# Optimization experiments

Measured on AMD Instinct MI355X. Metric: run time of the kernel, lower is better.

## Reference

```python
import jax, jax.numpy as jnp
import numpy as np

N = 32       # number of variables (per-var LSTMs)
L = 128      # window length
D = 128      # hidden dim
HEADS = 8
TAU_MAX = 5
ALPHA = 0.7  # attn_decay_alpha
B = 128      # number of time-ordered windows


def setup_inputs() -> dict:
    key = jax.random.key(0)
    ks = jax.random.split(key, 20)
    s = 0.1
    f = lambda k, shape: (jax.random.normal(k, shape, jnp.float32) * s)
    return {
        "X": jax.random.normal(ks[0], (B, L, N), jnp.float32),
        # per-variable encoder LSTM (input size 1): W_ih (N,4D), W_hh (N,4D,D), combined-style biases kept separate
        "enc_Wih": f(ks[1], (N, 4 * D)),
        "enc_Whh": f(ks[2], (N, 4 * D, D)),
        "enc_b": f(ks[3], (N, 4 * D)),            # b_ih + b_hh merged (mathematically identical)
        "pool_w": f(ks[4], (N, D)),
        "pool_b": f(ks[5], (N,)),
        # shared MultiheadAttention params (torch layout: in_proj (3D,D))
        "in_proj_w": f(ks[6], (3 * D, D)),
        "in_proj_b": f(ks[7], (3 * D,)),
        "out_proj_w": f(ks[8], (D, D)),
        "out_proj_b": f(ks[9], (D,)),
        # per-variable decoder: init_h/init_c Linear(d,d), LSTM(1,d) (input is all-zeros so W_ih drops out), out Linear(d,1)
        "dec_initH_w": f(ks[10], (N, D, D)),
        "dec_initH_b": f(ks[11], (N, D)),
        "dec_initC_w": f(ks[12], (N, D, D)),
        "dec_initC_b": f(ks[13], (N, D)),
        "dec_Whh": f(ks[14], (N, 4 * D, D)),
        "dec_bih": f(ks[15], (N, 4 * D)),
        "dec_bhh": f(ks[16], (N, 4 * D)),
        "dec_out_w": f(ks[17], (N, D)),
        "dec_out_b": f(ks[18], (N,)),
    }


def _lstm_cell(gates, c):
    # torch gate order: i, f, g, o
    i, fg, g, o = jnp.split(gates, 4, axis=-1)
    i = jax.nn.sigmoid(i); fg = jax.nn.sigmoid(fg)
    g = jnp.tanh(g); o = jax.nn.sigmoid(o)
    c = fg * c + i * g
    h = o * jnp.tanh(c)
    return h, c


def _encode(X, Wih, Whh, b, pool_w, pool_b):
    # X: (B,L,N); encoder consumes first L-1 steps of each variable, batched over all N vars
    x = jnp.transpose(X[:, :-1, :], (1, 2, 0))  # (T, N, B)
    Bn = X.shape[0]
    h0 = jnp.zeros((N, Bn, D), X.dtype)

    def step(carry, x_t):  # x_t: (N,B)
        h, c = carry
        gates = (x_t[..., None] * Wih[:, None, :]
                 + jnp.einsum('nbd,ngd->nbg', h, Whh)
                 + b[:, None, :])
        h, c = _lstm_cell(gates, c)
        return (h, c), h

    _, H = jax.lax.scan(step, (h0, h0), x)  # H: (T,N,B,D)
    # TemporalAttnPool: softmax over time of a linear score, weighted sum
    scores = jnp.einsum('tnbd,nd->tnb', H, pool_w) + pool_b[None, :, None]
    a = jax.nn.softmax(scores, axis=0)
    C = jnp.einsum('tnb,tnbd->bnd', a, H)  # (B,N,D)
    return C


def _mha(Q, KV, in_w, in_b, out_w, out_b):
    dh = D // HEADS
    q = Q @ in_w[:D].T + in_b[:D]
    k = KV @ in_w[D:2 * D].T + in_b[D:2 * D]
    v = KV @ in_w[2 * D:].T + in_b[2 * D:]
    sp = lambda x: x.reshape(x.shape[0], x.shape[1], HEADS, dh)
    q, k, v = sp(q), sp(k), sp(v)
    scores = jnp.einsum('bqhd,bkhd->bhqk', q, k) / float(np.sqrt(dh))
    attn = jax.nn.softmax(scores, axis=-1)
    o = jnp.einsum('bhqk,bkhd->bqhd', attn, v).reshape(Q.shape)
    return o @ out_w.T + out_b


def _cross_attend(C, in_w, in_b, out_w, out_b):
    Bn = C.shape[0]
    tmax = min(TAU_MAX, Bn - 1)
    if tmax <= 0:
        return C
    out_sum = jnp.zeros_like(C)
    w_sum = jnp.zeros((Bn, 1, 1), C.dtype)
    for tau in range(1, tmax + 1):  # small fixed loop over lags
        o = _mha(C[tau:], C[:-tau], in_w, in_b, out_w, out_b)
        w = float(np.exp(-ALPHA * (tau - 1)))  # attn_agg == 'decay'
        out_sum = out_sum.at[tau:].add(o * w)
        w_sum = w_sum.at[tau:].add(w)
    out = out_sum / jnp.clip(w_sum, 1e-8)
    return C + out  # residual=True


def _decode(C_star, iHw, iHb, iCw, iCb, Whh, bih, bhh, ow, ob):
    # h0/c0 from tanh(Linear(c_star)); LSTM input is all-zeros so input term reduces to b_ih
    h0 = jnp.tanh(jnp.einsum('bnd,ned->nbe', C_star, iHw) + iHb[:, None, :])
    c0 = jnp.tanh(jnp.einsum('bnd,ned->nbe', C_star, iCw) + iCb[:, None, :])
    b = (bih + bhh)[:, None, :]  # (N,1,4D)

    def step(carry, _):
        h, c = carry
        gates = jnp.einsum('nbd,ngd->nbg', h, Whh) + b
        h, c = _lstm_cell(gates, c)
        o = jnp.einsum('nbd,nd->nb', h, ow) + ob[:, None]
        return (h, c), o

    _, O = jax.lax.scan(step, (h0, c0), None, length=L)  # (L,N,B)
    recon = jnp.transpose(O[:L - 1], (2, 0, 1))  # (B,L-1,N)
    pred = O[L - 1].T                            # (B,N)
    return recon, pred


def reference(X, enc_Wih, enc_Whh, enc_b, pool_w, pool_b,
              in_proj_w, in_proj_b, out_proj_w, out_proj_b,
              dec_initH_w, dec_initH_b, dec_initC_w, dec_initC_b,
              dec_Whh, dec_bih, dec_bhh, dec_out_w, dec_out_b):
    C = _encode(X, enc_Wih, enc_Whh, enc_b, pool_w, pool_b)
    C_star = _cross_attend(C, in_proj_w, in_proj_b, out_proj_w, out_proj_b)
    recon, pred = _decode(C_star, dec_initH_w, dec_initH_b, dec_initC_w, dec_initC_b,
                          dec_Whh, dec_bih, dec_bhh, dec_out_w, dec_out_b)
    return recon, pred, C_star
```

## Files before the change

kernel.cpp:

```cpp
#include <hip/hip_runtime.h>
#include <hip/hip_bf16.h>

typedef unsigned short ushort_t;
typedef unsigned int uint_t;

#define DD   128
#define G4   512
#define BT   16
#define NB   128
#define NV   32

#define OFF_WIH   0
#define OFF_EB    16384
#define OFF_PW    32768
#define OFF_PB    36864
#define OFF_INW   37120
#define OFF_INB   86272
#define OFF_OUTW  86784
#define OFF_OUTB  103168
#define OFF_IHB   103424
#define OFF_ICB   107520
#define OFF_DBIH  111616
#define OFF_DBHH  128000
#define OFF_DOW   144384
#define OFF_DOB   148480
#define P_TOTAL   148736

typedef __attribute__((ext_vector_type(8))) short bf16x8;
typedef __attribute__((ext_vector_type(4))) float f32x4;

__device__ __forceinline__ float bf2f(ushort_t u) {
    union { uint_t i; float f; } x; x.i = ((uint_t)u) << 16; return x.f;
}
__device__ __forceinline__ ushort_t f2bf(float f) {
    __hip_bfloat16 h = __float2bfloat16(f);
    return *(ushort_t*)&h;
}
__device__ __forceinline__ uint_t f2u(float f) {
    union { float f; uint_t i; } x; x.f = f; return x.i;
}
__device__ __forceinline__ float u2f(uint_t u) {
    union { uint_t i; float f; } x; x.i = u; return x.f;
}
__device__ __forceinline__ float sigmoid_f(float x) {
    return __builtin_amdgcn_rcpf(1.f + __expf(-x));
}
__device__ __forceinline__ float tanh_f(float x) {
    float e = __expf(2.f * x);
    return 1.f - 2.f * __builtin_amdgcn_rcpf(e + 1.f);
}
__device__ __forceinline__ float swz_bcast_l15(float v) {
    return u2f((uint_t)__builtin_amdgcn_ds_swizzle((int)f2u(v), 0x000F));
}
__device__ __forceinline__ void store_out(void* out, long idx, float v, int bf) {
    if (bf) ((ushort_t*)out)[idx] = f2bf(v);
    else    ((float*)out)[idx]    = v;
}
__device__ __forceinline__ int wave_probe(const void* p, int elems) {
    int cap = elems < 2048 ? elems : 2048;
    int lane = threadIdx.x & 63;
    const ushort_t* u = (const ushort_t*)p;
    int cnt = 0, tot = 0;
    for (int j = lane; j < cap; j += 64) {
        ushort_t x = u[j];
        float af = fabsf(bf2f(x));
        tot++;
        if (x == 0 || (af > 1e-7f && af < 100.f)) cnt++;
    }
    #pragma unroll
    for (int off = 32; off >= 1; off >>= 1) {
        cnt += __shfl_xor(cnt, off);
        tot += __shfl_xor(tot, off);
    }
    return (cnt * 10 >= tot * 9) ? 1 : 0;
}

struct Ptr19 { const void* p[19]; };

__global__ __launch_bounds__(256) void prep_kernel(Ptr19 a, float* __restrict__ P,
                                                   float* __restrict__ Xc) {
    __shared__ float tile[32][65];
    if (blockIdx.x < 581) {
        int base = blockIdx.x * 256;
        int src, o0, size;
        if      (base < OFF_EB)   { src = 1;  o0 = base - OFF_WIH;  size = 16384; }
        else if (base < OFF_PW)   { src = 3;  o0 = base - OFF_EB;   size = 16384; }
        else if (base < OFF_PB)   { src = 4;  o0 = base - OFF_PW;   size = 4096;  }
        else if (base < OFF_INW)  { src = 5;  o0 = base - OFF_PB;   size = 32;    }
        else if (base < OFF_INB)  { src = 6;  o0 = base - OFF_INW;  size = 49152; }
        else if (base < OFF_OUTW) { src = 7;  o0 = base - OFF_INB;  size = 384;   }
        else if (base < OFF_OUTB) { src = 8;  o0 = base - OFF_OUTW; size = 16384; }
        else if (base < OFF_IHB)  { src = 9;  o0 = base - OFF_OUTB; size = 128;   }
        else if (base < OFF_ICB)  { src = 11; o0 = base - OFF_IHB;  size = 4096;  }
        else if (base < OFF_DBIH) { src = 13; o0 = base - OFF_ICB;  size = 4096;  }
        else if (base < OFF_DBHH) { src = 15; o0 = base - OFF_DBIH; size = 16384; }
        else if (base < OFF_DOW)  { src = 16; o0 = base - OFF_DBHH; size = 16384; }
        else if (base < OFF_DOB)  { src = 17; o0 = base - OFF_DOW;  size = 4096;  }
        else                      { src = 18; o0 = base - OFF_DOB;  size = 32;    }
        int bf = wave_probe(a.p[src], size);
        int off = o0 + (int)threadIdx.x;
        if (off < size)
            P[base + threadIdx.x] = bf ? bf2f(((const ushort_t*)a.p[src])[off])
                                       : ((const float*)a.p[src])[off];
    } else {
        int bf = wave_probe(a.p[0], 2048);
        int idx2 = blockIdx.x - 581;
        int bt = (idx2 & 3) * 32, tn0 = (idx2 >> 2) * 64;
        const void* src = a.p[0];
        int tx = threadIdx.x & 63, ty = threadIdx.x >> 6;
        #pragma unroll
        for (int k = 0; k < 8; k++) {
            int row = ty * 8 + k;
            int idx = (bt + row) * 4096 + tn0 + tx;
            tile[row][tx] = bf ? bf2f(((const ushort_t*)src)[idx]) : ((const float*)src)[idx];
        }
        __syncthreads();
        int bx = threadIdx.x & 31, tyy = threadIdx.x >> 5;
        #pragma unroll
        for (int k = 0; k < 8; k++) {
            int tn = tn0 + tyy * 8 + k;
            int t = tn >> 5, nn = tn & 31;
            Xc[t * 4096 + nn * 128 + bt + bx] = tile[bx][tyy * 8 + k];
        }
    }
}

__global__ __launch_bounds__(512, 2) void enc_kernel(
    const float* __restrict__ Xc, const void* __restrict__ Wraw,
    const float* __restrict__ P, float* __restrict__ Cout)
{
    const int n = blockIdx.y, b0 = blockIdx.x * BT;
    const int tid = threadIdx.x;
    const int w = tid >> 6, lane = tid & 63;
    const int l15 = lane & 15, quad = lane >> 4;
    const int wbf = wave_probe(Wraw, 2048);
    const int bown = b0 + l15;

    __shared__ alignas(16) ushort_t hS[2][16 * 136];
    for (int i = tid; i < 16 * 136; i += 512) hS[0][i] = 0;

    bf16x8 afrag[4][4];
    #pragma unroll
    for (int typ = 0; typ < 4; typ++) {
        const int g = typ * 128 + 16 * w + l15;
        #pragma unroll
        for (int kc = 0; kc < 4; kc++) {
            const int base = (n * G4 + g) * DD + 32 * kc + 8 * quad;
            if (wbf) {
                afrag[typ][kc] = *(const bf16x8*)((const ushort_t*)Wraw + base);
            } else {
                const float* fp = (const float*)Wraw + base;
                bf16x8 tmp;
                #pragma unroll
                for (int j = 0; j < 8; j++) tmp[j] = (short)f2bf(fp[j]);
                afrag[typ][kc] = tmp;
            }
        }
    }

    bf16x8 pfrag[4];
    #pragma unroll
    for (int kc = 0; kc < 4; kc++) {
        bf16x8 tmp;
        #pragma unroll
        for (int j = 0; j < 8; j++)
            tmp[j] = (l15 == 0 || l15 == 8)
                   ? (short)f2bf(P[OFF_PW + n * DD + 32 * kc + 8 * quad + j]) : (short)0;
        pfrag[kc] = tmp;
    }

    f32x4 bias4[4], wih4[4];
    #pragma unroll
    for (int typ = 0; typ < 4; typ++) {
        int base = n * G4 + typ * 128 + 16 * w + 4 * quad;
        bias4[typ] = *(const f32x4*)&P[OFF_EB + base];
        wih4[typ]  = *(const f32x4*)&P[OFF_WIH + base];
    }
    const float pb_r = P[OFF_PB + n];

    float cst[4], hprev[4], Cacc[4], lR = 0.f;
    #pragma unroll
    for (int r = 0; r < 4; r++) { cst[r] = 0.f; hprev[r] = 0.f; Cacc[r] = 0.f; }

    float xq = Xc[n * 128 + bown];

#define ENC_STEP(T, RB)                                                              \
    do {                                                                             \
        __syncthreads();                                                             \
        bf16x8 bh[4];                                                                \
        _Pragma("unroll")                                                            \
        for (int kc = 0; kc < 4; kc++)                                               \
            bh[kc] = *(const bf16x8*)&hS[RB][l15 * 136 + 32 * kc + 8 * quad];        \
        f32x4 acc[4], accP;                                                          \
        _Pragma("unroll")                                                            \
        for (int typ = 0; typ < 4; typ++) {                                          \
            f32x4 a;                                                                 \
            a.x = bias4[typ].x + xq * wih4[typ].x;                                   \
            a.y = bias4[typ].y + xq * wih4[typ].y;                                   \
            a.z = bias4[typ].z + xq * wih4[typ].z;                                   \
            a.w = bias4[typ].w + xq * wih4[typ].w;                                   \
            acc[typ] = a;                                                            \
        }                                                                            \
        accP.x = pb_r; accP.y = pb_r; accP.z = pb_r; accP.w = pb_r;                  \
        if ((T) < 126) xq = Xc[((T) + 1) * 4096 + n * 128 + bown];                   \
        _Pragma("unroll")                                                            \
        for (int kc = 0; kc < 4; kc++) {                                             \
            accP = __builtin_amdgcn_mfma_f32_16x16x32_bf16(pfrag[kc], bh[kc], accP, 0, 0, 0); \
            _Pragma("unroll")                                                        \
            for (int typ = 0; typ < 4; typ++)                                        \
                acc[typ] = __builtin_amdgcn_mfma_f32_16x16x32_bf16(afrag[typ][kc], bh[kc], acc[typ], 0, 0, 0); \
        }                                                                            \
        if ((T) > 0) {                                                               \
            float e = __expf(swz_bcast_l15(accP[0]));                                \
            lR += e;                                                                 \
            _Pragma("unroll")                                                        \
            for (int r = 0; r < 4; r++) Cacc[r] = fmaf(e, hprev[r], Cacc[r]);        \
        }                                                                            \
        ushort4 hw;                                                                  \
        _Pragma("unroll")                                                            \
        for (int r = 0; r < 4; r++) {                                                \
            float ii = sigmoid_f(acc[0][r]);                                         \
            float ff = sigmoid_f(acc[1][r]);                                         \
            float g2 = tanh_f(acc[2][r]);                                            \
            float oo = sigmoid_f(acc[3][r]);                                         \
            float cc = ff * cst[r] + ii * g2;                                        \
            cst[r] = cc;                                                             \
            float hh = oo * tanh_f(cc);                                              \
            hprev[r] = hh;                                                           \
            ((ushort_t*)&hw)[r] = f2bf(hh);                                          \
        }                                                                            \
        *(ushort4*)&hS[(RB) ^ 1][l15 * 136 + 16 * w + 4 * quad] = hw;                \
    } while (0)

    for (int tp = 0; tp < 63; tp++) {
        ENC_STEP(2 * tp, 0);
        ENC_STEP(2 * tp + 1, 1);
    }
    ENC_STEP(126, 0);
#undef ENC_STEP

    __syncthreads();
    {
        f32x4 accP;
        accP.x = pb_r; accP.y = pb_r; accP.z = pb_r; accP.w = pb_r;
        #pragma unroll
        for (int kc = 0; kc < 4; kc++) {
            bf16x8 bh = *(const bf16x8*)&hS[1][l15 * 136 + 32 * kc + 8 * quad];
            accP = __builtin_amdgcn_mfma_f32_16x16x32_bf16(pfrag[kc], bh, accP, 0, 0, 0);
        }
        float e = __expf(swz_bcast_l15(accP[0]));
        lR += e;
        #pragma unroll
        for (int r = 0; r < 4; r++) Cacc[r] = fmaf(e, hprev[r], Cacc[r]);
    }
    float inv = 1.f / lR;
    f32x4 cv;
    cv.x = Cacc[0] * inv; cv.y = Cacc[1] * inv; cv.z = Cacc[2] * inv; cv.w = Cacc[3] * inv;
    *(f32x4*)&Cout[bown * (NV * DD) + n * DD + 16 * w + 4 * quad] = cv;
}

__global__ __launch_bounds__(256) void qkv_kernel(
    const float* __restrict__ C, const float* __restrict__ P,
    float* __restrict__ q, float* __restrict__ k, float* __restrict__ v)
{
    int b = blockIdx.x, p = blockIdx.y, tid = threadIdx.x;
    int j = tid & 127, half = tid >> 7;
    __shared__ float Cb[NV * DD];
    for (int i = tid; i < NV * DD; i += 256) Cb[i] = C[b * (NV * DD) + i];
    __syncthreads();

    const float* wrow = P + OFF_INW + (p * DD + j) * DD;
    float bias = P[OFF_INB + p * DD + j];
    float acc[16];
    #pragma unroll
    for (int nn = 0; nn < 16; nn++) acc[nn] = bias;

    for (int dc = 0; dc < DD; dc += 8) {
        float4 w0 = *(const float4*)&wrow[dc];
        float4 w1 = *(const float4*)&wrow[dc + 4];
        #pragma unroll
        for (int nn = 0; nn < 16; nn++) {
            const float* cb = &Cb[(half * 16 + nn) * DD + dc];
            float4 c0 = *(float4*)&cb[0];
            float4 c1 = *(float4*)&cb[4];
            acc[nn] += c0.x * w0.x + c0.y * w0.y + c0.z * w0.z + c0.w * w0.w
                     + c1.x * w1.x + c1.y * w1.y + c1.z * w1.z + c1.w * w1.w;
        }
    }
    float* dst = (p == 0) ? q : (p == 1) ? k : v;
    for (int nn = 0; nn < 16; nn++)
        dst[b * (NV * DD) + (half * 16 + nn) * DD + j] = acc[nn];
}

__global__ __launch_bounds__(256) void attn_kernel(
    const float* __restrict__ q, const float* __restrict__ k, const float* __restrict__ v,
    const float* __restrict__ C, const float* __restrict__ P,
    const void* __restrict__ Xraw, float* __restrict__ Cstar, void* __restrict__ dout)
{
    int b = blockIdx.x, tid = threadIdx.x;
    int obf = wave_probe(Xraw, 2048);
    __shared__ float Qs[NV * DD], Ks[NV * DD], Vs[NV * DD];
    float* Os = Ks;
    for (int i = tid; i < NV * DD; i += 256) Qs[i] = q[b * (NV * DD) + i];
    __syncthreads();

    int hh = tid >> 5, qi = tid & 31;
    float qreg[16];
    #pragma unroll
    for (int u = 0; u < 4; u++) {
        float4 t4 = *(float4*)&Qs[qi * DD + hh * 16 + 4 * u];
        qreg[4*u] = t4.x; qreg[4*u+1] = t4.y; qreg[4*u+2] = t4.z; qreg[4*u+3] = t4.w;
    }

    float Oacc[16];
    #pragma unroll
    for (int u = 0; u < 16; u++) Oacc[u] = 0.f;
    float wsum = 0.f;
    int tmax = (b < 5) ? b : 5;

    for (int tau = 1; tau <= tmax; tau++) {
        __syncthreads();
        for (int i = tid; i < NV * DD; i += 256) {
            Ks[i] = k[(b - tau) * (NV * DD) + i];
            Vs[i] = v[(b - tau) * (NV * DD) + i];
        }
        __syncthreads();

        float s[NV];
        #pragma unroll
        for (int kk = 0; kk < NV; kk++) {
            float a = 0.f;
            #pragma unroll
            for (int u = 0; u < 4; u++) {
                float4 kv = *(float4*)&Ks[kk * DD + hh * 16 + 4 * u];
                a += qreg[4*u] * kv.x + qreg[4*u+1] * kv.y
                   + qreg[4*u+2] * kv.z + qreg[4*u+3] * kv.w;
            }
            s[kk] = a * 0.25f;
        }
        float mm = s[0];
        #pragma unroll
        for (int kk = 1; kk < NV; kk++) mm = fmaxf(mm, s[kk]);
        float ssum = 0.f;
        #pragma unroll
        for (int kk = 0; kk < NV; kk++) { s[kk] = __expf(s[kk] - mm); ssum += s[kk]; }
        float wdk = __expf(-0.7f * (float)(tau - 1));
        wsum += wdk;
        float wr = wdk / ssum;
        #pragma unroll
        for (int u = 0; u < 4; u++) {
            float ax = 0.f, ay = 0.f, az = 0.f, aw = 0.f;
            #pragma unroll
            for (int kk = 0; kk < NV; kk++) {
                float4 vv = *(float4*)&Vs[kk * DD + hh * 16 + 4 * u];
                ax += s[kk] * vv.x; ay += s[kk] * vv.y;
                az += s[kk] * vv.z; aw += s[kk] * vv.w;
            }
            Oacc[4*u] += wr * ax; Oacc[4*u+1] += wr * ay;
            Oacc[4*u+2] += wr * az; Oacc[4*u+3] += wr * aw;
        }
    }

    __syncthreads();
    float winv = (b > 0) ? 1.f / wsum : 0.f;
    #pragma unroll
    for (int u = 0; u < 16; u++)
        Os[qi * DD + hh * 16 + u] = Oacc[u] * winv;
    __syncthreads();

    int j = tid & 127, ng = tid >> 7;
    const float* wrow = P + OFF_OUTW + j * DD;
    float obias = P[OFF_OUTB + j];
    for (int nn = ng * 16; nn < ng * 16 + 16; nn++) {
        float a = (b > 0) ? obias : 0.f;
        for (int dc = 0; dc < DD; dc += 8) {
            float4 w0 = *(const float4*)&wrow[dc];
            float4 w1 = *(const float4*)&wrow[dc + 4];
            float4 o0 = *(float4*)&Os[nn * DD + dc];
            float4 o1 = *(float4*)&Os[nn * DD + dc + 4];
            a += o0.x*w0.x + o0.y*w0.y + o0.z*w0.z + o0.w*w0.w
               + o1.x*w1.x + o1.y*w1.y + o1.z*w1.z + o1.w*w1.w;
        }
        float cs = C[b * (NV * DD) + nn * DD + j] + a;
        Cstar[b * (NV * DD) + nn * DD + j] = cs;
        store_out(dout, 524288 + b * (NV * DD) + nn * DD + j, cs, obf);
    }
}

__global__ __launch_bounds__(512, 2) void dec_kernel(
    const float* __restrict__ Cstar,
    const void* __restrict__ iHw, const void* __restrict__ iCw,
    const void* __restrict__ Wraw, const void* __restrict__ Xraw,
    const float* __restrict__ P, void* __restrict__ out)
{
    const int n = blockIdx.y, b0 = blockIdx.x * BT;
    const int tid = threadIdx.x;
    const int w = tid >> 6, lane = tid & 63;
    const int l15 = lane & 15, quad = lane >> 4;
    const int wbf = wave_probe(Wraw, 2048);
    const int obf = wave_probe(Xraw, 2048);
    const int hbf = wave_probe(iHw, 2048);
    const int cbf = wave_probe(iCw, 2048);
    const int bown = b0 + l15;

    __shared__ alignas(16) ushort_t hS[2][16 * 136];

    bf16x8 cstB[4];
    #pragma unroll
    for (int kc = 0; kc < 4; kc++) {
        const float* cp = &Cstar[bown * (NV * DD) + n * DD + 32 * kc + 8 * quad];
        f32x4 c0v = *(const f32x4*)&cp[0];
        f32x4 c1v = *(const f32x4*)&cp[4];
        bf16x8 tmp;
        tmp[0] = (short)f2bf(c0v.x); tmp[1] = (short)f2bf(c0v.y);
        tmp[2] = (short)f2bf(c0v.z); tmp[3] = (short)f2bf(c0v.w);
        tmp[4] = (short)f2bf(c1v.x); tmp[5] = (short)f2bf(c1v.y);
        tmp[6] = (short)f2bf(c1v.z); tmp[7] = (short)f2bf(c1v.w);
        cstB[kc] = tmp;
    }
    float cst[4];
    {
        f32x4 hAcc = *(const f32x4*)&P[OFF_IHB + n * DD + 16 * w + 4 * quad];
        f32x4 cAcc = *(const f32x4*)&P[OFF_ICB + n * DD + 16 * w + 4 * quad];
        #pragma unroll
        for (int kc = 0; kc < 4; kc++) {
            const int base = (n * DD + 16 * w + l15) * DD + 32 * kc + 8 * quad;
            bf16x8 wA;
            if (hbf) wA = *(const bf16x8*)((const ushort_t*)iHw + base);
            else {
                const float* fp = (const float*)iHw + base;
                #pragma unroll
                for (int j = 0; j < 8; j++) wA[j] = (short)f2bf(fp[j]);
            }
            hAcc = __builtin_amdgcn_mfma_f32_16x16x32_bf16(wA, cstB[kc], hAcc, 0, 0, 0);
            if (cbf) wA = *(const bf16x8*)((const ushort_t*)iCw + base);
            else {
                const float* fp = (const float*)iCw + base;
                #pragma unroll
                for (int j = 0; j < 8; j++) wA[j] = (short)f2bf(fp[j]);
            }
            cAcc = __builtin_amdgcn_mfma_f32_16x16x32_bf16(wA, cstB[kc], cAcc, 0, 0, 0);
        }
        ushort4 hw;
        #pragma unroll
        for (int r = 0; r < 4; r++) {
            ((ushort_t*)&hw)[r] = f2bf(tanh_f(hAcc[r]));
            cst[r] = tanh_f(cAcc[r]);
        }
        *(ushort4*)&hS[0][l15 * 136 + 16 * w + 4 * quad] = hw;
    }

    bf16x8 afrag[4][4];
    #pragma unroll
    for (int typ = 0; typ < 4; typ++) {
        const int g = typ * 128 + 16 * w + l15;
        #pragma unroll
        for (int kc = 0; kc < 4; kc++) {
            const int base = (n * G4 + g) * DD + 32 * kc + 8 * quad;
            if (wbf) {
                afrag[typ][kc] = *(const bf16x8*)((const ushort_t*)Wraw + base);
            } else {
                const float* fp = (const float*)Wraw + base;
                bf16x8 tmp;
                #pragma unroll
                for (int j = 0; j < 8; j++) tmp[j] = (short)f2bf(fp[j]);
                afrag[typ][kc] = tmp;
            }
        }
    }

    bf16x8 pfrag[4];
    #pragma unroll
    for (int kc = 0; kc < 4; kc++) {
        bf16x8 tmp;
        #pragma unroll
        for (int j = 0; j < 8; j++)
            tmp[j] = (l15 == 0) ? (short)f2bf(P[OFF_DOW + n * DD + 32 * kc + 8 * quad + j]) : (short)0;
        pfrag[kc] = tmp;
    }

    f32x4 bias4[4];
    #pragma unroll
    for (int typ = 0; typ < 4; typ++) {
        int base = n * G4 + typ * 128 + 16 * w + 4 * quad;
        f32x4 b1 = *(const f32x4*)&P[OFF_DBIH + base];
        f32x4 b2 = *(const f32x4*)&P[OFF_DBHH + base];
        bias4[typ].x = b1.x + b2.x; bias4[typ].y = b1.y + b2.y;
        bias4[typ].z = b1.z + b2.z; bias4[typ].w = b1.w + b2.w;
    }
    const float ob_r = P[OFF_DOB + n];

#define DEC_STEP(T, RB)                                                              \
    do {                                                                             \
        __syncthreads();                                                             \
        bf16x8 bh[4];                                                                \
        _Pragma("unroll")                                                            \
        for (int kc = 0; kc < 4; kc++)                                               \
            bh[kc] = *(const bf16x8*)&hS[RB][l15 * 136 + 32 * kc + 8 * quad];        \
        f32x4 acc[4];                                                                \
        _Pragma("unroll")                                                            \
        for (int typ = 0; typ < 4; typ++) acc[typ] = bias4[typ];                     \
        _Pragma("unroll")                                                            \
        for (int kc = 0; kc < 4; kc++)                                               \
            _Pragma("unroll")                                                        \
            for (int typ = 0; typ < 4; typ++)                                        \
                acc[typ] = __builtin_amdgcn_mfma_f32_16x16x32_bf16(afrag[typ][kc], bh[kc], acc[typ], 0, 0, 0); \
        if (w == 0) {                                                                \
            f32x4 accP;                                                              \
            accP.x = ob_r; accP.y = ob_r; accP.z = ob_r; accP.w = ob_r;              \
            _Pragma("unroll")                                                        \
            for (int kc = 0; kc < 4; kc++)                                           \
                accP = __builtin_amdgcn_mfma_f32_16x16x32_bf16(pfrag[kc], bh[kc], accP, 0, 0, 0); \
            if ((T) > 0 && quad == 0)                                                \
                store_out(out, (long)bown * 4064 + (long)((T) - 1) * NV + n, accP[0], obf); \
        }                                                                            \
        ushort4 hw;                                                                  \
        _Pragma("unroll")                                                            \
        for (int r = 0; r < 4; r++) {                                                \
            float ii = sigmoid_f(acc[0][r]);                                         \
            float ff = sigmoid_f(acc[1][r]);                                         \
            float g2 = tanh_f(acc[2][r]);                                            \
            float oo = sigmoid_f(acc[3][r]);                                         \
            float cc = ff * cst[r] + ii * g2;                                        \
            cst[r] = cc;                                                             \
            ((ushort_t*)&hw)[r] = f2bf(oo * tanh_f(cc));                             \
        }                                                                            \
        *(ushort4*)&hS[(RB) ^ 1][l15 * 136 + 16 * w + 4 * quad] = hw;                \
    } while (0)

    for (int tp = 0; tp < 64; tp++) {
        DEC_STEP(2 * tp, 0);
        DEC_STEP(2 * tp + 1, 1);
    }
#undef DEC_STEP

    __syncthreads();
    if (w == 0) {
        f32x4 accP;
        accP.x = ob_r; accP.y = ob_r; accP.z = ob_r; accP.w = ob_r;
        #pragma unroll
        for (int kc = 0; kc < 4; kc++) {
            bf16x8 bh = *(const bf16x8*)&hS[0][l15 * 136 + 32 * kc + 8 * quad];
            accP = __builtin_amdgcn_mfma_f32_16x16x32_bf16(pfrag[kc], bh, accP, 0, 0, 0);
        }
        if (quad == 0)
            store_out(out, 520192 + (long)bown * NV + n, accP[0], obf);
    }
}

extern "C" void kernel_launch(void* const* d_in, const int* in_sizes, int n_in,
                              void* d_out, int out_size, void* d_ws, size_t ws_size,
                              hipStream_t stream) {
    char* ws = (char*)d_ws;
    float*    P    = (float*)(ws + 0);
    float*    Xc   = (float*)(ws + (1u << 20));
    float*    C    = (float*)(ws + (3u << 20));
    float*    qb   = (float*)(ws + (5u << 20));
    float*    kb   = (float*)(ws + (7u << 20));
    float*    vb   = (float*)(ws + (9u << 20));
    float*    Cst  = (float*)(ws + (11u << 20));

    Ptr19 a;
    for (int i = 0; i < 19; i++) a.p[i] = d_in[i];

    prep_kernel<<<837, 256, 0, stream>>>(a, P, Xc);
    enc_kernel<<<dim3(8, 32), 512, 0, stream>>>(Xc, d_in[2], P, C);
    qkv_kernel<<<dim3(128, 3), 256, 0, stream>>>(C, P, qb, kb, vb);
    attn_kernel<<<128, 256, 0, stream>>>(qb, kb, vb, C, P, d_in[0], Cst, d_out);
    dec_kernel<<<dim3(8, 32), 512, 0, stream>>>(Cst, d_in[10], d_in[12], d_in[14], d_in[0], P, d_out);
}
```

Measured before the change: 436.1 us.

## Split MFMA accumulation chains and precompute dtype flags in prep kernel

The recurrent gate matmuls in the encoder and decoder now accumulate into two independent register chains (k-chunks 0-1 and 2-3) that are summed at the end. This shortens the dependent MFMA chain on the per-step critical path. The dtype probes that each block used to run on entry are computed once by five extra prep blocks and stored as flags in P. The pooling weight fragment is now replicated across all rows, so the swizzle broadcast of the attention logit can be dropped. The cost is extra accumulator registers and a few vector adds per step.

After: 448.4 us. 1.03x slower.

```diff
diff --git a/kernel.cpp b/kernel.cpp
--- a/kernel.cpp
+++ b/kernel.cpp
@@ -25,6 +25,7 @@
 #define OFF_DOW   144384
 #define OFF_DOB   148480
 #define P_TOTAL   148736
+#define OFF_FLAGS (OFF_PB + 32)
 
 typedef __attribute__((ext_vector_type(8))) short bf16x8;
 typedef __attribute__((ext_vector_type(4))) float f32x4;
@@ -36,21 +37,12 @@
     __hip_bfloat16 h = __float2bfloat16(f);
     return *(ushort_t*)&h;
 }
-__device__ __forceinline__ uint_t f2u(float f) {
-    union { float f; uint_t i; } x; x.f = f; return x.i;
-}
-__device__ __forceinline__ float u2f(uint_t u) {
-    union { uint_t i; float f; } x; x.i = u; return x.f;
-}
 __device__ __forceinline__ float sigmoid_f(float x) {
     return __builtin_amdgcn_rcpf(1.f + __expf(-x));
 }
 __device__ __forceinline__ float tanh_f(float x) {
     float e = __expf(2.f * x);
     return 1.f - 2.f * __builtin_amdgcn_rcpf(e + 1.f);
-}
-__device__ __forceinline__ float swz_bcast_l15(float v) {
-    return u2f((uint_t)__builtin_amdgcn_ds_swizzle((int)f2u(v), 0x000F));
 }
 __device__ __forceinline__ void store_out(void* out, long idx, float v, int bf) {
     if (bf) ((ushort_t*)out)[idx] = f2bf(v);
@@ -102,7 +94,7 @@
         if (off < size)
             P[base + threadIdx.x] = bf ? bf2f(((const ushort_t*)a.p[src])[off])
                                        : ((const float*)a.p[src])[off];
-    } else {
+    } else if (blockIdx.x < 837) {
         int bf = wave_probe(a.p[0], 2048);
         int idx2 = blockIdx.x - 581;
         int bt = (idx2 & 3) * 32, tn0 = (idx2 >> 2) * 64;
@@ -122,6 +114,12 @@
             int t = tn >> 5, nn = tn & 31;
             Xc[t * 4096 + nn * 128 + bt + bx] = tile[bx][tyy * 8 + k];
         }
+    } else {
+        int which = blockIdx.x - 837;
+        int src = (which == 0) ? 0 : (which == 1) ? 2 : (which == 2) ? 10
+                : (which == 3) ? 12 : 14;
+        int flag = wave_probe(a.p[src], 2048);
+        if (threadIdx.x == 0) P[OFF_FLAGS + which] = (float)flag;
     }
 }
 
@@ -133,7 +131,7 @@
     const int tid = threadIdx.x;
     const int w = tid >> 6, lane = tid & 63;
     const int l15 = lane & 15, quad = lane >> 4;
-    const int wbf = wave_probe(Wraw, 2048);
+    const int wbf = P[OFF_FLAGS + 1] > 0.5f;
     const int bown = b0 + l15;
 
     __shared__ alignas(16) ushort_t hS[2][16 * 136];
@@ -164,8 +162,7 @@
         bf16x8 tmp;
         #pragma unroll
         for (int j = 0; j < 8; j++)
-            tmp[j] = (l15 == 0 || l15 == 8)
-                   ? (short)f2bf(P[OFF_PW + n * DD + 32 * kc + 8 * quad + j]) : (short)0;
+            tmp[j] = (short)f2bf(P[OFF_PW + n * DD + 32 * kc + 8 * quad + j]);
         pfrag[kc] = tmp;
     }
 
@@ -191,7 +188,7 @@
         _Pragma("unroll")                                                            \
         for (int kc = 0; kc < 4; kc++)                                               \
             bh[kc] = *(const bf16x8*)&hS[RB][l15 * 136 + 32 * kc + 8 * quad];        \
-        f32x4 acc[4], accP;                                                          \
+        f32x4 acc[4], acc2[4], accP, accP2;                                          \
         _Pragma("unroll")                                                            \
         for (int typ = 0; typ < 4; typ++) {                                          \
             f32x4 a;                                                                 \
@@ -200,18 +197,29 @@
             a.z = bias4[typ].z + xq * wih4[typ].z;                                   \
             a.w = bias4[typ].w + xq * wih4[typ].w;                                   \
             acc[typ] = a;                                                            \
+            acc2[typ].x = 0.f; acc2[typ].y = 0.f; acc2[typ].z = 0.f; acc2[typ].w = 0.f; \
         }                                                                            \
         accP.x = pb_r; accP.y = pb_r; accP.z = pb_r; accP.w = pb_r;                  \
+        accP2.x = 0.f; accP2.y = 0.f; accP2.z = 0.f; accP2.w = 0.f;                  \
         if ((T) < 126) xq = Xc[((T) + 1) * 4096 + n * 128 + bown];                   \
         _Pragma("unroll")                                                            \
-        for (int kc = 0; kc < 4; kc++) {                                             \
+        for (int kc = 0; kc < 2; kc++) {                                             \
             accP = __builtin_amdgcn_mfma_f32_16x16x32_bf16(pfrag[kc], bh[kc], accP, 0, 0, 0); \
             _Pragma("unroll")                                                        \
             for (int typ = 0; typ < 4; typ++)                                        \
                 acc[typ] = __builtin_amdgcn_mfma_f32_16x16x32_bf16(afrag[typ][kc], bh[kc], acc[typ], 0, 0, 0); \
         }                                                                            \
+        _Pragma("unroll")                                                            \
+        for (int kc = 2; kc < 4; kc++) {                                             \
+            accP2 = __builtin_amdgcn_mfma_f32_16x16x32_bf16(pfrag[kc], bh[kc], accP2, 0, 0, 0); \
+            _Pragma("unroll")                                                        \
+            for (int typ = 0; typ < 4; typ++)                                        \
+                acc2[typ] = __builtin_amdgcn_mfma_f32_16x16x32_bf16(afrag[typ][kc], bh[kc], acc2[typ], 0, 0, 0); \
+        }                                                                            \
+        _Pragma("unroll")                                                            \
+        for (int typ = 0; typ < 4; typ++) acc[typ] = acc[typ] + acc2[typ];           \
         if ((T) > 0) {                                                               \
-            float e = __expf(swz_bcast_l15(accP[0]));                                \
+            float e = __expf(accP[0] + accP2[0]);                                    \
             lR += e;                                                                 \
             _Pragma("unroll")                                                        \
             for (int r = 0; r < 4; r++) Cacc[r] = fmaf(e, hprev[r], Cacc[r]);        \
@@ -248,7 +256,7 @@
             bf16x8 bh = *(const bf16x8*)&hS[1][l15 * 136 + 32 * kc + 8 * quad];
             accP = __builtin_amdgcn_mfma_f32_16x16x32_bf16(pfrag[kc], bh, accP, 0, 0, 0);
         }
-        float e = __expf(swz_bcast_l15(accP[0]));
+        float e = __expf(accP[0]);
         lR += e;
         #pragma unroll
         for (int r = 0; r < 4; r++) Cacc[r] = fmaf(e, hprev[r], Cacc[r]);
@@ -295,10 +303,10 @@
 __global__ __launch_bounds__(256) void attn_kernel(
     const float* __restrict__ q, const float* __restrict__ k, const float* __restrict__ v,
     const float* __restrict__ C, const float* __restrict__ P,
-    const void* __restrict__ Xraw, float* __restrict__ Cstar, void* __restrict__ dout)
+    float* __restrict__ Cstar, void* __restrict__ dout)
 {
     int b = blockIdx.x, tid = threadIdx.x;
-    int obf = wave_probe(Xraw, 2048);
+    int obf = P[OFF_FLAGS + 0] > 0.5f;
     __shared__ float Qs[NV * DD], Ks[NV * DD], Vs[NV * DD];
     float* Os = Ks;
     for (int i = tid; i < NV * DD; i += 256) Qs[i] = q[b * (NV * DD) + i];
@@ -390,17 +398,17 @@
 __global__ __launch_bounds__(512, 2) void dec_kernel(
     const float* __restrict__ Cstar,
     const void* __restrict__ iHw, const void* __restrict__ iCw,
-    const void* __restrict__ Wraw, const void* __restrict__ Xraw,
+    const void* __restrict__ Wraw,
     const float* __restrict__ P, void* __restrict__ out)
 {
     const int n = blockIdx.y, b0 = blockIdx.x * BT;
     const int tid = threadIdx.x;
     const int w = tid >> 6, lane = tid & 63;
     const int l15 = lane & 15, quad = lane >> 4;
-    const int wbf = wave_probe(Wraw, 2048);
-    const int obf = wave_probe(Xraw, 2048);
-    const int hbf = wave_probe(iHw, 2048);
-    const int cbf = wave_probe(iCw, 2048);
+    const int obf = P[OFF_FLAGS + 0] > 0.5f;
+    const int hbf = P[OFF_FLAGS + 2] > 0.5f;
+    const int cbf = P[OFF_FLAGS + 3] > 0.5f;
+    const int wbf = P[OFF_FLAGS + 4] > 0.5f;
     const int bown = b0 + l15;
 
     __shared__ alignas(16) ushort_t hS[2][16 * 136];
@@ -497,14 +505,24 @@
         _Pragma("unroll")                                                            \
         for (int kc = 0; kc < 4; kc++)                                               \
             bh[kc] = *(const bf16x8*)&hS[RB][l15 * 136 + 32 * kc + 8 * quad];        \
-        f32x4 acc[4];                                                                \
-        _Pragma("unroll")                                                            \
-        for (int typ = 0; typ < 4; typ++) acc[typ] = bias4[typ];                     \
-        _Pragma("unroll")                                                            \
-        for (int kc = 0; kc < 4; kc++)                                               \
+        f32x4 acc[4], acc2[4];                                                       \
+        _Pragma("unroll")                                                            \
+        for (int typ = 0; typ < 4; typ++) {                                          \
+            acc[typ] = bias4[typ];                                                   \
+            acc2[typ].x = 0.f; acc2[typ].y = 0.f; acc2[typ].z = 0.f; acc2[typ].w = 0.f; \
+        }                                                                            \
+        _Pragma("unroll")                                                            \
+        for (int kc = 0; kc < 2; kc++)                                               \
             _Pragma("unroll")                                                        \
             for (int typ = 0; typ < 4; typ++)                                        \
                 acc[typ] = __builtin_amdgcn_mfma_f32_16x16x32_bf16(afrag[typ][kc], bh[kc], acc[typ], 0, 0, 0); \
+        _Pragma("unroll")                                                            \
+        for (int kc = 2; kc < 4; kc++)                                               \
+            _Pragma("unroll")                                                        \
+            for (int typ = 0; typ < 4; typ++)                                        \
+                acc2[typ] = __builtin_amdgcn_mfma_f32_16x16x32_bf16(afrag[typ][kc], bh[kc], acc2[typ], 0, 0, 0); \
+        _Pragma("unroll")                                                            \
+        for (int typ = 0; typ < 4; typ++) acc[typ] = acc[typ] + acc2[typ];           \
         if (w == 0) {                                                                \
             f32x4 accP;                                                              \
             accP.x = ob_r; accP.y = ob_r; accP.z = ob_r; accP.w = ob_r;              \
@@ -563,9 +581,9 @@
     Ptr19 a;
     for (int i = 0; i < 19; i++) a.p[i] = d_in[i];
 
-    prep_kernel<<<837, 256, 0, stream>>>(a, P, Xc);
+    prep_kernel<<<842, 256, 0, stream>>>(a, P, Xc);
     enc_kernel<<<dim3(8, 32), 512, 0, stream>>>(Xc, d_in[2], P, C);
     qkv_kernel<<<dim3(128, 3), 256, 0, stream>>>(C, P, qb, kb, vb);
-    attn_kernel<<<128, 256, 0, stream>>>(qb, kb, vb, C, P, d_in[0], Cst, d_out);
-    dec_kernel<<<dim3(8, 32), 512, 0, stream>>>(Cst, d_in[10], d_in[12], d_in[14], d_in[0], P, d_out);
-}
+    attn_kernel<<<128, 256, 0, stream>>>(qb, kb, vb, C, P, Cst, d_out);
+    dec_kernel<<<dim3(8, 32), 512, 0, stream>>>(Cst, d_in[10], d_in[12], d_in[14], P, d_out);
+}
```

## Precompute dtype probe flags once and split attention across query halves

Applied to the files above, without the earlier changes.

Adds five blocks to the prep kernel that run the bf16/fp32 dtype probe once per input and store the flags in padding inside the parameter buffer. Encoder, attention and decoder read these flags instead of each probing the input again. Attention now launches two blocks of 128 threads per window, each handling 16 query variables, which doubles the block count for more parallelism. The cost is that both blocks reload the full K/V tiles, and correctness depends on the flag slots not overlapping real parameter data.

Result: faster. 427.3 us (-2.0%).

```diff
diff --git a/kernel.cpp b/kernel.cpp
--- a/kernel.cpp
+++ b/kernel.cpp
@@ -25,6 +25,7 @@
 #define OFF_DOW   144384
 #define OFF_DOB   148480
 #define P_TOTAL   148736
+#define OFF_FLAGS (OFF_PB + 32)
 
 typedef __attribute__((ext_vector_type(8))) short bf16x8;
 typedef __attribute__((ext_vector_type(4))) float f32x4;
@@ -102,7 +103,7 @@
         if (off < size)
             P[base + threadIdx.x] = bf ? bf2f(((const ushort_t*)a.p[src])[off])
                                        : ((const float*)a.p[src])[off];
-    } else {
+    } else if (blockIdx.x < 837) {
         int bf = wave_probe(a.p[0], 2048);
         int idx2 = blockIdx.x - 581;
         int bt = (idx2 & 3) * 32, tn0 = (idx2 >> 2) * 64;
@@ -122,6 +123,12 @@
             int t = tn >> 5, nn = tn & 31;
             Xc[t * 4096 + nn * 128 + bt + bx] = tile[bx][tyy * 8 + k];
         }
+    } else {
+        int which = blockIdx.x - 837;
+        int src = (which == 0) ? 0 : (which == 1) ? 2 : (which == 2) ? 10
+                : (which == 3) ? 12 : 14;
+        int flag = wave_probe(a.p[src], 2048);
+        if (threadIdx.x == 0) P[OFF_FLAGS + which] = (float)flag;
     }
 }
 
@@ -133,7 +140,7 @@
     const int tid = threadIdx.x;
     const int w = tid >> 6, lane = tid & 63;
     const int l15 = lane & 15, quad = lane >> 4;
-    const int wbf = wave_probe(Wraw, 2048);
+    const int wbf = P[OFF_FLAGS + 1] > 0.5f;
     const int bown = b0 + l15;
 
     __shared__ alignas(16) ushort_t hS[2][16 * 136];
@@ -292,19 +299,20 @@
         dst[b * (NV * DD) + (half * 16 + nn) * DD + j] = acc[nn];
 }
 
-__global__ __launch_bounds__(256) void attn_kernel(
+__global__ __launch_bounds__(128) void attn_kernel(
     const float* __restrict__ q, const float* __restrict__ k, const float* __restrict__ v,
     const float* __restrict__ C, const float* __restrict__ P,
-    const void* __restrict__ Xraw, float* __restrict__ Cstar, void* __restrict__ dout)
+    float* __restrict__ Cstar, void* __restrict__ dout)
 {
-    int b = blockIdx.x, tid = threadIdx.x;
-    int obf = wave_probe(Xraw, 2048);
-    __shared__ float Qs[NV * DD], Ks[NV * DD], Vs[NV * DD];
+    int b = blockIdx.x, half = blockIdx.y, tid = threadIdx.x;
+    int obf = P[OFF_FLAGS + 0] > 0.5f;
+    int n0 = half * 16;
+    __shared__ float Qs[16 * DD], Ks[NV * DD], Vs[NV * DD];
     float* Os = Ks;
-    for (int i = tid; i < NV * DD; i += 256) Qs[i] = q[b * (NV * DD) + i];
+    for (int i = tid; i < 16 * DD; i += 128) Qs[i] = q[b * (NV * DD) + n0 * DD + i];
     __syncthreads();
 
-    int hh = tid >> 5, qi = tid & 31;
+    int hh = tid >> 4, qi = tid & 15;
     float qreg[16];
     #pragma unroll
     for (int u = 0; u < 4; u++) {
@@ -320,7 +328,7 @@
 
     for (int tau = 1; tau <= tmax; tau++) {
         __syncthreads();
-        for (int i = tid; i < NV * DD; i += 256) {
+        for (int i = tid; i < NV * DD; i += 128) {
             Ks[i] = k[(b - tau) * (NV * DD) + i];
             Vs[i] = v[(b - tau) * (NV * DD) + i];
         }
@@ -368,10 +376,10 @@
         Os[qi * DD + hh * 16 + u] = Oacc[u] * winv;
     __syncthreads();
 
-    int j = tid & 127, ng = tid >> 7;
+    int j = tid;
     const float* wrow = P + OFF_OUTW + j * DD;
     float obias = P[OFF_OUTB + j];
-    for (int nn = ng * 16; nn < ng * 16 + 16; nn++) {
+    for (int nn = 0; nn < 16; nn++) {
         float a = (b > 0) ? obias : 0.f;
         for (int dc = 0; dc < DD; dc += 8) {
             float4 w0 = *(const float4*)&wrow[dc];
@@ -381,26 +389,27 @@
             a += o0.x*w0.x + o0.y*w0.y + o0.z*w0.z + o0.w*w0.w
                + o1.x*w1.x + o1.y*w1.y + o1.z*w1.z + o1.w*w1.w;
         }
-        float cs = C[b * (NV * DD) + nn * DD + j] + a;
-        Cstar[b * (NV * DD) + nn * DD + j] = cs;
-        store_out(dout, 524288 + b * (NV * DD) + nn * DD + j, cs, obf);
+        int nng = n0 + nn;
+        float cs = C[b * (NV * DD) + nng * DD + j] + a;
+        Cstar[b * (NV * DD) + nng * DD + j] = cs;
+        store_out(dout, 524288 + b * (NV * DD) + nng * DD + j, cs, obf);
     }
 }
 
 __global__ __launch_bounds__(512, 2) void dec_kernel(
     const float* __restrict__ Cstar,
     const void* __restrict__ iHw, const void* __restrict__ iCw,
-    const void* __restrict__ Wraw, const void* __restrict__ Xraw,
+    const void* __restrict__ Wraw,
     const float* __restrict__ P, void* __restrict__ out)
 {
     const int n = blockIdx.y, b0 = blockIdx.x * BT;
     const int tid = threadIdx.x;
     const int w = tid >> 6, lane = tid & 63;
     const int l15 = lane & 15, quad = lane >> 4;
-    const int wbf = wave_probe(Wraw, 2048);
-    const int obf = wave_probe(Xraw, 2048);
-    const int hbf = wave_probe(iHw, 2048);
-    const int cbf = wave_probe(iCw, 2048);
+    const int obf = P[OFF_FLAGS + 0] > 0.5f;
+    const int hbf = P[OFF_FLAGS + 2] > 0.5f;
+    const int cbf = P[OFF_FLAGS + 3] > 0.5f;
+    const int wbf = P[OFF_FLAGS + 4] > 0.5f;
     const int bown = b0 + l15;
 
     __shared__ alignas(16) ushort_t hS[2][16 * 136];
@@ -563,9 +572,9 @@
     Ptr19 a;
     for (int i = 0; i < 19; i++) a.p[i] = d_in[i];
 
-    prep_kernel<<<837, 256, 0, stream>>>(a, P, Xc);
+    prep_kernel<<<842, 256, 0, stream>>>(a, P, Xc);
     enc_kernel<<<dim3(8, 32), 512, 0, stream>>>(Xc, d_in[2], P, C);
     qkv_kernel<<<dim3(128, 3), 256, 0, stream>>>(C, P, qb, kb, vb);
-    attn_kernel<<<128, 256, 0, stream>>>(qb, kb, vb, C, P, d_in[0], Cst, d_out);
-    dec_kernel<<<dim3(8, 32), 512, 0, stream>>>(Cst, d_in[10], d_in[12], d_in[14], d_in[0], P, d_out);
-}
+    attn_kernel<<<dim3(128, 2), 128, 0, stream>>>(qb, kb, vb, C, P, Cst, d_out);
+    dec_kernel<<<dim3(8, 32), 512, 0, stream>>>(Cst, d_in[10], d_in[12], d_in[14], P, d_out);
+}
```
